# Kernel tuning notes

Measured on AMD Instinct MI355X. Metric: run time of the kernel, lower is better.

Reference implementation:

```python
import jax, jax.numpy as jnp
import numpy as np


def _rope(x, C):
    # x: [B, H, W, C]; 2 spatial channel dims -> k_max = C // 4
    B, H, W, _ = x.shape
    k_max = C // 4
    theta = 1.0 / (10000.0 ** (jnp.arange(k_max, dtype=x.dtype) / k_max))
    hh, ww = jnp.meshgrid(jnp.arange(H, dtype=x.dtype), jnp.arange(W, dtype=x.dtype), indexing='ij')
    angles = jnp.concatenate([hh[..., None] * theta, ww[..., None] * theta], axis=-1)  # [H, W, C//2]
    cos, sin = jnp.cos(angles), jnp.sin(angles)
    xr = x.reshape(B, H, W, C // 2, 2)
    x_re, x_im = xr[..., 0], xr[..., 1]
    out = jnp.stack([x_re * cos - x_im * sin, x_im * cos + x_re * sin], axis=-1)
    return out.reshape(B, H, W, C)


def _forward(x, W_qk, b_qk, scale_p, dwc_w, dwc_b, img_H, img_W):
    B, N, C = x.shape
    head_dim = dwc_w.shape[0]
    h = C // head_dim
    f = 3  # focusing_factor

    qk = x @ W_qk.T + b_qk                        # [B, N, 2C]
    q, k = qk[..., :C], qk[..., C:]
    v = x

    q = _rope(q.reshape(B, img_H, img_W, C), C).reshape(B, N, C)
    k = _rope(k.reshape(B, img_H, img_W, C), C).reshape(B, N, C)

    q = jax.nn.elu(q) + 1.0
    k = jax.nn.elu(k) + 1.0

    scale = jax.nn.softplus(scale_p)              # [1, 1, C]
    q = q / scale
    k = k / scale

    q_norm = jnp.linalg.norm(q, axis=-1, keepdims=True)
    k_norm = jnp.linalg.norm(k, axis=-1, keepdims=True)
    q = q ** f
    k = k ** f
    q = q / jnp.linalg.norm(q, axis=-1, keepdims=True) * q_norm
    k = k / jnp.linalg.norm(k, axis=-1, keepdims=True) * k_norm

    q = q.reshape(B, N, h, head_dim).transpose(0, 2, 1, 3)   # [B, h, N, d]
    k = k.reshape(B, N, h, head_dim).transpose(0, 2, 1, 3)
    v = v.reshape(B, N, h, head_dim).transpose(0, 2, 1, 3)

    k_mean = k.mean(axis=2, keepdims=True)                    # [B, h, 1, d]
    z = 1.0 / (jnp.einsum('bhnd,bhmd->bhnm', q, k_mean) + 1e-6)  # [B, h, N, 1]

    s = float(N) ** (-0.5)
    kv = jnp.einsum('bhnd,bhne->bhde', k * s, v * s)          # [B, h, d, d]
    out = jnp.einsum('bhnd,bhde->bhne', q, kv) * z            # [B, h, N, d]
    out = out.transpose(0, 2, 1, 3).reshape(B, N, C)

    # depthwise conv residual on v
    v_img = v.reshape(B * h, img_H, img_W, head_dim).transpose(0, 3, 1, 2)  # [B*h, d, H, W]
    conv = jax.lax.conv_general_dilated(
        v_img, dwc_w, window_strides=(1, 1), padding='SAME',
        dimension_numbers=('NCHW', 'OIHW', 'NCHW'),
        feature_group_count=head_dim) + dwc_b[None, :, None, None]
    out = out + conv.reshape(B, C, N).transpose(0, 2, 1)
    return out


def setup_inputs() -> dict:
    key = jax.random.key(0)
    ks = jax.random.split(key, 6)
    B, img_H, img_W, C, head_dim, ksz = 8, 64, 64, 512, 32, 5
    N = img_H * img_W
    x = jax.random.normal(ks[0], (B, N, C), dtype=jnp.float32)
    W_qk = jax.random.normal(ks[1], (2 * C, C), dtype=jnp.float32) * 0.02
    b_qk = jnp.zeros((2 * C,), dtype=jnp.float32)
    scale_p = jax.random.normal(ks[2], (1, 1, C), dtype=jnp.float32) * 0.02
    fan_out = ksz * ksz  # depthwise: out_channels/groups = 1
    dwc_w = jax.random.normal(ks[3], (head_dim, 1, ksz, ksz), dtype=jnp.float32) * np.sqrt(2.0 / fan_out)
    dwc_b = jnp.zeros((head_dim,), dtype=jnp.float32)
    return {"x": x, "W_qk": W_qk, "b_qk": b_qk, "scale_p": scale_p,
            "dwc_w": dwc_w, "dwc_b": dwc_b, "img_H": img_H, "img_W": img_W}


def reference(x, W_qk, b_qk, scale_p, dwc_w, dwc_b, img_H, img_W):
    return _forward(x, W_qk, b_qk, scale_p, dwc_w, dwc_b, img_H, img_W)
```

## Files before the change

kernel.cpp:

```cpp
#include <hip/hip_runtime.h>
#include <math.h>

#define B_SZ 8
#define IMG_H 64
#define IMG_W 64
#define N_TOK 4096
#define C_DIM 512
#define HEADS 16
#define HDIM 32
#define M_ROWS (B_SZ * N_TOK)
#define QK_COLS (2 * C_DIM)

#define THETA_COEF (-0.07195578415606394f)

typedef __attribute__((ext_vector_type(8))) __bf16 bf16x8;
typedef __attribute__((ext_vector_type(4))) float f32x4;

__device__ __forceinline__ void async_ld16(void* lds, const void* g) {
    __builtin_amdgcn_global_load_lds(
        (const __attribute__((address_space(1))) unsigned*)g,
        (__attribute__((address_space(3))) unsigned*)lds, 16, 0, 0);
}

__device__ __forceinline__ unsigned short f2bf(float f) {
    unsigned u = __float_as_uint(f);
    u += 0x7FFF + ((u >> 16) & 1);
    return (unsigned short)(u >> 16);
}

__global__ __launch_bounds__(256) void cvt_bf16_kernel(
    const float* __restrict__ src, unsigned short* __restrict__ dst)
{
    int i = blockIdx.x * 256 + threadIdx.x;
    float4 v = ((const float4*)src)[i];
    ushort4 o;
    o.x = f2bf(v.x); o.y = f2bf(v.y); o.z = f2bf(v.z); o.w = f2bf(v.w);
    ((ushort4*)dst)[i] = o;
}

__global__ __launch_bounds__(256) void rope_lut_kernel(
    const float* __restrict__ scale_p, float* __restrict__ lut)
{
    int idx = blockIdx.x * 256 + threadIdx.x;
    int pos = idx >> 7, tt = idx & 127;
    float theta = expf((float)tt * THETA_COEF);
    float ang = (float)pos * theta;
    lut[idx] = cosf(ang);
    lut[idx + 8192] = sinf(ang);
    if (idx < 512) lut[16384 + idx] = 1.0f / log1pf(expf(scale_p[idx]));
}

#define GBM 128
#define GBN 128
#define GBK 64

#define EPI_I(I, ACC) do {                                                    \
    float cr = cI, sr = sI;                                                   \
    _Pragma("unroll")                                                         \
    for (int r = 0; r < 4; ++r) {                                             \
        int m = m0 + wm + (I) * 16 + quad * 4 + r;                            \
        float val = (ACC)[r] + bias;                                          \
        float oth = __shfl_xor(val, 1);                                       \
        float rot = is_im ? (val * cr + oth * sr) : (val * cr - oth * sr);    \
        rot = (rot > 0.f) ? (rot + 1.f) : __expf(rot);                        \
        dst[(size_t)m * C_DIM + ch] = rot * rspv;                             \
        float tc = cr * c1 - sr * s1, ts = sr * c1 + cr * s1;                 \
        cr = tc; sr = ts;                                                     \
    }                                                                         \
    float uc = cI * c16 - sI * s16, us = sI * c16 + cI * s16;                 \
    cI = uc; sI = us;                                                         \
} while (0)

#define EPI_J(J, A0, A1, A2, A3) do {                                         \
    int c = n0 + wn + (J) * 16 + l16;                                         \
    int ch = c & 511;                                                         \
    float bias = bqk[c];                                                      \
    float rspv = rsp[ch];                                                     \
    int tt = ch >> 1;                                                         \
    int tl = tt & 127;                                                        \
    float cI, sI, c1, s1, c16, s16;                                           \
    if (tt < 128) {               \
        int pos = ((m0 + wm) & (N_TOK - 1)) >> 6;                             \
        cI = lut[pos * 128 + tl]; sI = lut[pos * 128 + tl + 8192];            \
        c1 = 1.f; s1 = 0.f; c16 = 1.f; s16 = 0.f;                             \
    } else {                  \
        int pos0 = quad * 4;                                                  \
        cI = lut[pos0 * 128 + tl]; sI = lut[pos0 * 128 + tl + 8192];          \
        c1  = lut[128 + tl];       s1  = lut[128 + tl + 8192];                \
        c16 = lut[2048 + tl];      s16 = lut[2048 + tl + 8192];               \
    }                                                                         \
    float* dst = (c < C_DIM) ? qW : kW;                                       \
    EPI_I(0, A0); EPI_I(1, A1); EPI_I(2, A2); EPI_I(3, A3);                   \
} while (0)

__global__ __launch_bounds__(256, 1) void gemm_mfma_kernel(
    const unsigned short* __restrict__ xb,
    const unsigned short* __restrict__ Wb,
    const float* __restrict__ bqk,
    const float* __restrict__ lut,
    float* __restrict__ qW,
    float* __restrict__ kW)
{
    __shared__ char lds[32768];
    char* As = lds;
    char* Bs = lds + 16384;

    const float* rsp = lut + 16384;

    const int t = threadIdx.x;
    const int wave = t >> 6;
    const int lane = t & 63;
    const int quad = lane >> 4;
    const int l16 = lane & 15;
    const int is_im = l16 & 1;

    const int flat = blockIdx.x + 8 * blockIdx.y;
    const int xcd = flat & 7;
    const int ii_ = flat >> 3;
    const int n0 = (ii_ & 7) * GBN;
    const int m0 = (xcd * 32 + (ii_ >> 3)) * GBM;

    const int wm = (wave >> 1) * 64;
    const int wn = (wave & 1) * 64;

    const int sr_ = t >> 3;
    const int ss_ = t & 7;

    f32x4 acc00 = {0.f,0.f,0.f,0.f}, acc01 = {0.f,0.f,0.f,0.f},
          acc02 = {0.f,0.f,0.f,0.f}, acc03 = {0.f,0.f,0.f,0.f},
          acc10 = {0.f,0.f,0.f,0.f}, acc11 = {0.f,0.f,0.f,0.f},
          acc12 = {0.f,0.f,0.f,0.f}, acc13 = {0.f,0.f,0.f,0.f},
          acc20 = {0.f,0.f,0.f,0.f}, acc21 = {0.f,0.f,0.f,0.f},
          acc22 = {0.f,0.f,0.f,0.f}, acc23 = {0.f,0.f,0.f,0.f},
          acc30 = {0.f,0.f,0.f,0.f}, acc31 = {0.f,0.f,0.f,0.f},
          acc32 = {0.f,0.f,0.f,0.f}, acc33 = {0.f,0.f,0.f,0.f};

    const int swz = (l16 >> 1) & 3;
    const int par = l16 & 1;

    for (int k0 = 0; k0 < C_DIM; k0 += GBK) {
        __syncthreads();
#pragma unroll
        for (int p = 0; p < 2; ++p) {
#pragma unroll
            for (int qq = 0; qq < 2; ++qq) {
                int r = qq * 32 + sr_;
                int j = ((ss_ & 3) ^ ((r >> 1) & 3)) | ((ss_ & 4) ^ ((r & 1) << 2));
                const unsigned short* ga =
                    xb + (size_t)(m0 + p * 64 + r) * C_DIM + k0 + j * 8;
                async_ld16(As + p * 8192 + qq * 4096 + wave * 1024, ga);
                const unsigned short* gb =
                    Wb + (size_t)(n0 + p * 64 + r) * C_DIM + k0 + j * 8;
                async_ld16(Bs + p * 8192 + qq * 4096 + wave * 1024, gb);
            }
        }
        __syncthreads();

#pragma unroll
        for (int kk = 0; kk < 2; ++kk) {
            const int co = ((quad ^ swz) + 4 * (kk ^ par)) * 16;
            bf16x8 a0 = *(const bf16x8*)(As + (wm + 0 * 16 + l16) * 128 + co);
            bf16x8 a1 = *(const bf16x8*)(As + (wm + 1 * 16 + l16) * 128 + co);
            bf16x8 a2 = *(const bf16x8*)(As + (wm + 2 * 16 + l16) * 128 + co);
            bf16x8 a3 = *(const bf16x8*)(As + (wm + 3 * 16 + l16) * 128 + co);
            bf16x8 b0 = *(const bf16x8*)(Bs + (wn + 0 * 16 + l16) * 128 + co);
            bf16x8 b1 = *(const bf16x8*)(Bs + (wn + 1 * 16 + l16) * 128 + co);
            bf16x8 b2 = *(const bf16x8*)(Bs + (wn + 2 * 16 + l16) * 128 + co);
            bf16x8 b3 = *(const bf16x8*)(Bs + (wn + 3 * 16 + l16) * 128 + co);

            acc00 = __builtin_amdgcn_mfma_f32_16x16x32_bf16(a0, b0, acc00, 0, 0, 0);
            acc01 = __builtin_amdgcn_mfma_f32_16x16x32_bf16(a0, b1, acc01, 0, 0, 0);
            acc02 = __builtin_amdgcn_mfma_f32_16x16x32_bf16(a0, b2, acc02, 0, 0, 0);
            acc03 = __builtin_amdgcn_mfma_f32_16x16x32_bf16(a0, b3, acc03, 0, 0, 0);
            acc10 = __builtin_amdgcn_mfma_f32_16x16x32_bf16(a1, b0, acc10, 0, 0, 0);
            acc11 = __builtin_amdgcn_mfma_f32_16x16x32_bf16(a1, b1, acc11, 0, 0, 0);
            acc12 = __builtin_amdgcn_mfma_f32_16x16x32_bf16(a1, b2, acc12, 0, 0, 0);
            acc13 = __builtin_amdgcn_mfma_f32_16x16x32_bf16(a1, b3, acc13, 0, 0, 0);
            acc20 = __builtin_amdgcn_mfma_f32_16x16x32_bf16(a2, b0, acc20, 0, 0, 0);
            acc21 = __builtin_amdgcn_mfma_f32_16x16x32_bf16(a2, b1, acc21, 0, 0, 0);
            acc22 = __builtin_amdgcn_mfma_f32_16x16x32_bf16(a2, b2, acc22, 0, 0, 0);
            acc23 = __builtin_amdgcn_mfma_f32_16x16x32_bf16(a2, b3, acc23, 0, 0, 0);
            acc30 = __builtin_amdgcn_mfma_f32_16x16x32_bf16(a3, b0, acc30, 0, 0, 0);
            acc31 = __builtin_amdgcn_mfma_f32_16x16x32_bf16(a3, b1, acc31, 0, 0, 0);
            acc32 = __builtin_amdgcn_mfma_f32_16x16x32_bf16(a3, b2, acc32, 0, 0, 0);
            acc33 = __builtin_amdgcn_mfma_f32_16x16x32_bf16(a3, b3, acc33, 0, 0, 0);
        }
    }

    EPI_J(0, acc00, acc10, acc20, acc30);
    EPI_J(1, acc01, acc11, acc21, acc31);
    EPI_J(2, acc02, acc12, acc22, acc32);
    EPI_J(3, acc03, acc13, acc23, acc33);
}

__global__ __launch_bounds__(256) void norm_kernel(
    const float* __restrict__ qW, const float* __restrict__ kW,
    float* __restrict__ sq, float* __restrict__ sk)
{
    int wave = threadIdx.x >> 6;
    int lane = threadIdx.x & 63;
    int m = blockIdx.x * 4 + wave;
    const float4* qr = (const float4*)(qW + (size_t)m * C_DIM);
    const float4* kr = (const float4*)(kW + (size_t)m * C_DIM);
    float q2 = 0.f, q6 = 0.f, k2 = 0.f, k6 = 0.f;
#pragma unroll
    for (int l = 0; l < 2; ++l) {
        float4 q4 = qr[lane + l * 64];
        float4 k4 = kr[lane + l * 64];
        float qq;
        qq = q4.x * q4.x; q2 += qq; q6 += qq * qq * qq;
        qq = q4.y * q4.y; q2 += qq; q6 += qq * qq * qq;
        qq = q4.z * q4.z; q2 += qq; q6 += qq * qq * qq;
        qq = q4.w * q4.w; q2 += qq; q6 += qq * qq * qq;
        qq = k4.x * k4.x; k2 += qq; k6 += qq * qq * qq;
        qq = k4.y * k4.y; k2 += qq; k6 += qq * qq * qq;
        qq = k4.z * k4.z; k2 += qq; k6 += qq * qq * qq;
        qq = k4.w * k4.w; k2 += qq; k6 += qq * qq * qq;
    }
#pragma unroll
    for (int off = 32; off > 0; off >>= 1) {
        q2 += __shfl_down(q2, off);
        q6 += __shfl_down(q6, off);
        k2 += __shfl_down(k2, off);
        k6 += __shfl_down(k6, off);
    }
    if (lane == 0) {
        sq[m] = sqrtf(q2) / sqrtf(q6);
        sk[m] = sqrtf(k2) / sqrtf(k6);
    }
}

#define NSPLIT 8
#define ROWS_PER_SPLIT (N_TOK / NSPLIT)

__global__ __launch_bounds__(256) void kv_partial_kernel(
    const float* __restrict__ x, const float* __restrict__ kW,
    const float* __restrict__ sk,
    float* __restrict__ kvp, float* __restrict__ kmp)
{
    int g = blockIdx.x >> 3;
    int split = blockIdx.x & 7;
    int b = g >> 4, h = g & 15;
    int n_start = split * ROWS_PER_SPLIT;

    __shared__ float smem[5120];
    float* kf = smem;
    float* vv = smem + 64 * 36;

    int t = threadIdx.x;
    int wave = t >> 6, lane = t & 63;
    int srow = t >> 3;
    int scol = (t & 7) * 4;
    int d0 = (lane >> 3) * 4;
    int e0 = (lane & 7) * 4;

    float acc[4][4] = {{0.f}};
    float4 kmacc = make_float4(0.f, 0.f, 0.f, 0.f);

    float4 kreg[2], vreg[2];
    float sreg[2];
#pragma unroll
    for (int h2 = 0; h2 < 2; ++h2) {
        int n = n_start + h2 * 32 + srow;
        size_t base = ((size_t)(b * N_TOK + n)) * C_DIM + h * HDIM + scol;
        kreg[h2] = *(const float4*)&kW[base];
        vreg[h2] = *(const float4*)&x[base];
        sreg[h2] = sk[b * N_TOK + n];
    }

    for (int tt = 0; tt < ROWS_PER_SPLIT / 64; ++tt) {
        __syncthreads();
#pragma unroll
        for (int h2 = 0; h2 < 2; ++h2) {
            int row = h2 * 32 + srow;
            float4 k4 = kreg[h2];
            float s = sreg[h2];
            float4 k3;
            k3.x = k4.x * k4.x * k4.x * s;
            k3.y = k4.y * k4.y * k4.y * s;
            k3.z = k4.z * k4.z * k4.z * s;
            k3.w = k4.w * k4.w * k4.w * s;
            *(float4*)&kf[row * 36 + scol] = k3;
            *(float4*)&vv[row * 36 + scol] = vreg[h2];
            kmacc.x += k3.x; kmacc.y += k3.y;
            kmacc.z += k3.z; kmacc.w += k3.w;
        }
        if (tt < ROWS_PER_SPLIT / 64 - 1) {
            int nb = n_start + (tt + 1) * 64;
#pragma unroll
            for (int h2 = 0; h2 < 2; ++h2) {
                int n = nb + h2 * 32 + srow;
                size_t base = ((size_t)(b * N_TOK + n)) * C_DIM + h * HDIM + scol;
                kreg[h2] = *(const float4*)&kW[base];
                vreg[h2] = *(const float4*)&x[base];
                sreg[h2] = sk[b * N_TOK + n];
            }
        }
        __syncthreads();

        const float* kfp = kf + (wave * 16) * 36 + d0;
        const float* vvp = vv + (wave * 16) * 36 + e0;
#pragma unroll
        for (int nn = 0; nn < 16; ++nn) {
            float4 k4 = *(const float4*)(kfp + nn * 36);
            float4 v4 = *(const float4*)(vvp + nn * 36);
            acc[0][0] += k4.x * v4.x; acc[0][1] += k4.x * v4.y;
            acc[0][2] += k4.x * v4.z; acc[0][3] += k4.x * v4.w;
            acc[1][0] += k4.y * v4.x; acc[1][1] += k4.y * v4.y;
            acc[1][2] += k4.y * v4.z; acc[1][3] += k4.y * v4.w;
            acc[2][0] += k4.z * v4.x; acc[2][1] += k4.z * v4.y;
            acc[2][2] += k4.z * v4.z; acc[2][3] += k4.z * v4.w;
            acc[3][0] += k4.w * v4.x; acc[3][1] += k4.w * v4.y;
            acc[3][2] += k4.w * v4.z; acc[3][3] += k4.w * v4.w;
        }
    }

    __syncthreads();
    float* red = smem;
    float* kmr = smem + 4096;
#pragma unroll
    for (int di = 0; di < 4; ++di) {
        float4 v = make_float4(acc[di][0], acc[di][1], acc[di][2], acc[di][3]);
        *(float4*)&red[wave * 1024 + (d0 + di) * 32 + e0] = v;
    }
    *(float4*)&kmr[srow * 32 + scol] = kmacc;
    __syncthreads();

    size_t pbase = (size_t)blockIdx.x * 1024;
    for (int idx = t; idx < 1024; idx += 256) {
        float s = red[idx] + red[1024 + idx] + red[2048 + idx] + red[3072 + idx];
        kvp[pbase + idx] = s;
    }
    if (t < 32) {
        float s = 0.f;
#pragma unroll
        for (int r = 0; r < 32; ++r) s += kmr[r * 32 + t];
        kmp[blockIdx.x * 32 + t] = s;
    }
}

__global__ __launch_bounds__(256) void kv_reduce_kernel(
    const float* __restrict__ kvp, const float* __restrict__ kmp,
    float* __restrict__ kv, float* __restrict__ km)
{
    int g = blockIdx.x;
    int t = threadIdx.x;
    for (int idx = t; idx < 1024; idx += 256) {
        float s = 0.f;
#pragma unroll
        for (int sp = 0; sp < NSPLIT; ++sp)
            s += kvp[((size_t)(g * NSPLIT + sp)) * 1024 + idx];
        int d = idx >> 5, e = idx & 31;
        kv[(size_t)g * 1024 + e * 32 + d] = s * (1.0f / 4096.0f);
    }
    if (t < 32) {
        float s = 0.f;
#pragma unroll
        for (int sp = 0; sp < NSPLIT; ++sp) s += kmp[(g * NSPLIT + sp) * 32 + t];
        km[g * 32 + t] = s * (1.0f / 4096.0f);
    }
}

__global__ __launch_bounds__(256) void attn_out_kernel(
    const float* __restrict__ qW, const float* __restrict__ sq,
    const float* __restrict__ kvT, const float* __restrict__ km,
    float* __restrict__ out)
{
    int g = blockIdx.x;
    int b = g >> 4, h = g & 15;
    int n0 = blockIdx.y * 128;

    __shared__ float qf[16][36];

    int t = threadIdx.x;
    int e = t & 15;
    int nl = t >> 4;
    int sd = e * 2;

    const float* kvg = kvT + (size_t)g * 1024;
    float4 kva[8], kvb[8], kmr[8];
#pragma unroll
    for (int j = 0; j < 8; ++j) {
        kva[j] = *(const float4*)&kvg[e * 32 + j * 4];
        kvb[j] = *(const float4*)&kvg[(e + 16) * 32 + j * 4];
        kmr[j] = *(const float4*)&km[g * 32 + j * 4];
    }

    size_t rbase = ((size_t)(b * N_TOK + n0 + nl)) * C_DIM + h * HDIM;

    float2 q2 = *(const float2*)&qW[rbase + sd];
    float sv = sq[b * N_TOK + n0 + nl];

    for (int ch = 0; ch < 8; ++ch) {
        __syncthreads();
        *(float2*)&qf[nl][sd] =
            make_float2(q2.x * q2.x * q2.x * sv, q2.y * q2.y * q2.y * sv);

        float2 q2n; float svn;
        if (ch < 7) {
            size_t nb = rbase + (size_t)(ch + 1) * 16 * C_DIM;
            q2n = *(const float2*)&qW[nb + sd];
            svn = sq[b * N_TOK + n0 + (ch + 1) * 16 + nl];
        }
        __syncthreads();

        float s1a = 0.f, s1b = 0.f, s2 = 0.f;
#pragma unroll
        for (int j = 0; j < 8; ++j) {
            float4 q4 = *(const float4*)&qf[nl][j * 4];
            s1a += q4.x * kva[j].x + q4.y * kva[j].y
                 + q4.z * kva[j].z + q4.w * kva[j].w;
            s1b += q4.x * kvb[j].x + q4.y * kvb[j].y
                 + q4.z * kvb[j].z + q4.w * kvb[j].w;
            s2  += q4.x * kmr[j].x + q4.y * kmr[j].y
                 + q4.z * kmr[j].z + q4.w * kmr[j].w;
        }
        float z = 1.0f / (s2 + 1e-6f);
        float* op = out + rbase + (size_t)ch * 16 * C_DIM;
        op[e] = s1a * z;
        op[e + 16] = s1b * z;

        if (ch < 7) { q2 = q2n; sv = svn; }
    }
}

__global__ __launch_bounds__(256, 2) void conv_kernel(
    const float* __restrict__ x, const float* __restrict__ w,
    const float* __restrict__ bias, float* __restrict__ out)
{
    __shared__ float wl[25][32];
    int t = threadIdx.x;
    for (int idx = t; idx < 800; idx += 256) {
        int o = idx & 31, tap = idx >> 5;
        wl[tap][o] = w[o * 25 + tap];
    }
    __syncthreads();

    int bi = blockIdx.x >> 3;
    int part = blockIdx.x & 7;
    int b = bi >> 6, i = bi & 63;
    int jg = part * 2 + (t >> 7);
    int cg = t & 127;
    int j0 = jg * 4;
    int o4 = (cg & 7) * 4;

    const float* xbase = x + ((size_t)b * N_TOK) * C_DIM + cg * 4;

    float4 b4 = *(const float4*)&bias[o4];
    float4 acc[4] = {b4, b4, b4, b4};

#pragma unroll
    for (int ki = 0; ki < 5; ++ki) {
        int ii = i + ki - 2;
        if (ii < 0 || ii >= IMG_H) continue;
        const float* xr = xbase + (size_t)ii * 64 * C_DIM;
        float4 row[8];
#pragma unroll
        for (int jx = 0; jx < 8; ++jx) {
            int jj = j0 + jx - 2;
            row[jx] = (jj >= 0 && jj < IMG_W)
                          ? *(const float4*)(xr + (size_t)jj * C_DIM)
                          : make_float4(0.f, 0.f, 0.f, 0.f);
        }
#pragma unroll
        for (int kj = 0; kj < 5; ++kj) {
            float4 w4 = *(const float4*)&wl[ki * 5 + kj][o4];
#pragma unroll
            for (int jo = 0; jo < 4; ++jo) {
                acc[jo].x += w4.x * row[jo + kj].x;
                acc[jo].y += w4.y * row[jo + kj].y;
                acc[jo].z += w4.z * row[jo + kj].z;
                acc[jo].w += w4.w * row[jo + kj].w;
            }
        }
    }

    float* op = out + ((size_t)(b * N_TOK + i * 64 + j0)) * C_DIM + cg * 4;
#pragma unroll
    for (int jo = 0; jo < 4; ++jo) {
        float4 cur = *(float4*)(op + (size_t)jo * C_DIM);
        cur.x += acc[jo].x;
        cur.y += acc[jo].y;
        cur.z += acc[jo].z;
        cur.w += acc[jo].w;
        *(float4*)(op + (size_t)jo * C_DIM) = cur;
    }
}

extern "C" void kernel_launch(void* const* d_in, const int* in_sizes, int n_in,
                              void* d_out, int out_size, void* d_ws, size_t ws_size,
                              hipStream_t stream) {
    const float* x       = (const float*)d_in[0];
    const float* Wqk     = (const float*)d_in[1];
    const float* bqk     = (const float*)d_in[2];
    const float* scale_p = (const float*)d_in[3];
    const float* dwc_w   = (const float*)d_in[4];
    const float* dwc_b   = (const float*)d_in[5];
    float* out = (float*)d_out;
    float* ws = (float*)d_ws;

    float* qW  = ws;
    float* sq  = qW + (size_t)M_ROWS * C_DIM;
    float* sk  = sq + M_ROWS;
    float* kvp = sk + M_ROWS;
    float* kmp = kvp + (size_t)1024 * 1024;
    float* kv  = kmp + 1024 * 32;
    float* km  = kv + 128 * 1024;
    unsigned short* xb = (unsigned short*)(km + 2048);
    unsigned short* Wb = xb + (size_t)M_ROWS * C_DIM;
    float* lut = (float*)(Wb + (size_t)QK_COLS * C_DIM);
    float* kW  = out;

    cvt_bf16_kernel<<<(M_ROWS * C_DIM) / 1024, 256, 0, stream>>>(x, xb);
    cvt_bf16_kernel<<<(QK_COLS * C_DIM) / 1024, 256, 0, stream>>>(Wqk, Wb);
    rope_lut_kernel<<<32, 256, 0, stream>>>(scale_p, lut);

    dim3 gg(QK_COLS / GBN, M_ROWS / GBM);
    gemm_mfma_kernel<<<gg, 256, 0, stream>>>(xb, Wb, bqk, lut, qW, kW);

    norm_kernel<<<M_ROWS / 4, 256, 0, stream>>>(qW, kW, sq, sk);

    kv_partial_kernel<<<128 * NSPLIT, 256, 0, stream>>>(x, kW, sk, kvp, kmp);
    kv_reduce_kernel<<<128, 256, 0, stream>>>(kvp, kmp, kv, km);

    dim3 g4(128, 32);
    attn_out_kernel<<<g4, 256, 0, stream>>>(qW, sq, kv, km, out);

    conv_kernel<<<M_ROWS / 8, 256, 0, stream>>>(x, dwc_w, dwc_b, out);
}
```

Baseline: 338.9 us.

## Double-buffer GEMM LDS tiles with GBK=32 and merge prep kernels

Rewrites the QK GEMM main loop to ping-pong between two 16KB LDS buffers of K-depth 32, so the async global-to-LDS load for the next tile is issued before the MFMAs on the current tile. This needs one barrier per iteration instead of two. Separately, the two bf16 conversion launches and the RoPE LUT launch are merged into one prep kernel to save launch overhead. The cost is twice as many loop iterations, each with less MFMA work to hide latency behind, plus a different LDS swizzle.

```diff
diff --git a/kernel.cpp b/kernel.cpp
--- a/kernel.cpp
+++ b/kernel.cpp
@@ -28,31 +28,40 @@
     return (unsigned short)(u >> 16);
 }
 
-__global__ __launch_bounds__(256) void cvt_bf16_kernel(
-    const float* __restrict__ src, unsigned short* __restrict__ dst)
-{
-    int i = blockIdx.x * 256 + threadIdx.x;
-    float4 v = ((const float4*)src)[i];
-    ushort4 o;
-    o.x = f2bf(v.x); o.y = f2bf(v.y); o.z = f2bf(v.z); o.w = f2bf(v.w);
-    ((ushort4*)dst)[i] = o;
-}
-
-__global__ __launch_bounds__(256) void rope_lut_kernel(
-    const float* __restrict__ scale_p, float* __restrict__ lut)
-{
-    int idx = blockIdx.x * 256 + threadIdx.x;
-    int pos = idx >> 7, tt = idx & 127;
-    float theta = expf((float)tt * THETA_COEF);
-    float ang = (float)pos * theta;
-    lut[idx] = cosf(ang);
-    lut[idx + 8192] = sinf(ang);
-    if (idx < 512) lut[16384 + idx] = 1.0f / log1pf(expf(scale_p[idx]));
+__global__ __launch_bounds__(256) void prep_kernel(
+    const float* __restrict__ x, const float* __restrict__ Wqk,
+    const float* __restrict__ scale_p,
+    unsigned short* __restrict__ xb, unsigned short* __restrict__ Wb,
+    float* __restrict__ lut)
+{
+    int bid = blockIdx.x;
+    int t = threadIdx.x;
+    if (bid < 16384) {
+        int i = bid * 256 + t;
+        float4 v = ((const float4*)x)[i];
+        ushort4 o;
+        o.x = f2bf(v.x); o.y = f2bf(v.y); o.z = f2bf(v.z); o.w = f2bf(v.w);
+        ((ushort4*)xb)[i] = o;
+    } else if (bid < 16896) {
+        int i = (bid - 16384) * 256 + t;
+        float4 v = ((const float4*)Wqk)[i];
+        ushort4 o;
+        o.x = f2bf(v.x); o.y = f2bf(v.y); o.z = f2bf(v.z); o.w = f2bf(v.w);
+        ((ushort4*)Wb)[i] = o;
+    } else {
+        int idx = (bid - 16896) * 256 + t;
+        int pos = idx >> 7, tt = idx & 127;
+        float theta = expf((float)tt * THETA_COEF);
+        float ang = (float)pos * theta;
+        lut[idx] = cosf(ang);
+        lut[idx + 8192] = sinf(ang);
+        if (idx < 512) lut[16384 + idx] = 1.0f / log1pf(expf(scale_p[idx]));
+    }
 }
 
 #define GBM 128
 #define GBN 128
-#define GBK 64
+#define GBK 32
 
 #define EPI_I(I, ACC) do {                                                    \
     float cr = cI, sr = sI;                                                   \
@@ -102,8 +111,6 @@
     float* __restrict__ kW)
 {
     __shared__ char lds[32768];
-    char* As = lds;
-    char* Bs = lds + 16384;
 
     const float* rsp = lut + 16384;
 
@@ -123,8 +130,8 @@
     const int wm = (wave >> 1) * 64;
     const int wn = (wave & 1) * 64;
 
-    const int sr_ = t >> 3;
-    const int ss_ = t & 7;
+    const int srow = t >> 2;
+    const int sj = t & 3;
 
     f32x4 acc00 = {0.f,0.f,0.f,0.f}, acc01 = {0.f,0.f,0.f,0.f},
           acc02 = {0.f,0.f,0.f,0.f}, acc03 = {0.f,0.f,0.f,0.f},
@@ -136,55 +143,57 @@
           acc32 = {0.f,0.f,0.f,0.f}, acc33 = {0.f,0.f,0.f,0.f};
 
     const int swz = (l16 >> 1) & 3;
-    const int par = l16 & 1;
+    const int co = (quad ^ swz) * 16;
+
+    auto stage = [&](int k0, int b) {
+#pragma unroll
+        for (int p = 0; p < 2; ++p) {
+            int m = p * 64 + srow;
+            int jp = sj ^ ((m >> 1) & 3);
+            const unsigned short* ga = xb + (size_t)(m0 + m) * C_DIM + k0 + jp * 8;
+            async_ld16(lds + b * 16384 + p * 4096 + wave * 1024, ga);
+            const unsigned short* gb = Wb + (size_t)(n0 + m) * C_DIM + k0 + jp * 8;
+            async_ld16(lds + b * 16384 + 8192 + p * 4096 + wave * 1024, gb);
+        }
+    };
+
+    stage(0, 0);
+    __syncthreads();
+    int buf = 0;
 
     for (int k0 = 0; k0 < C_DIM; k0 += GBK) {
+        if (k0 + GBK < C_DIM) stage(k0 + GBK, buf ^ 1);
+
+        const char* As = lds + buf * 16384;
+        const char* Bs = As + 8192;
+        bf16x8 a0 = *(const bf16x8*)(As + (wm + 0 * 16 + l16) * 64 + co);
+        bf16x8 a1 = *(const bf16x8*)(As + (wm + 1 * 16 + l16) * 64 + co);
+        bf16x8 a2 = *(const bf16x8*)(As + (wm + 2 * 16 + l16) * 64 + co);
+        bf16x8 a3 = *(const bf16x8*)(As + (wm + 3 * 16 + l16) * 64 + co);
+        bf16x8 b0 = *(const bf16x8*)(Bs + (wn + 0 * 16 + l16) * 64 + co);
+        bf16x8 b1 = *(const bf16x8*)(Bs + (wn + 1 * 16 + l16) * 64 + co);
+        bf16x8 b2 = *(const bf16x8*)(Bs + (wn + 2 * 16 + l16) * 64 + co);
+        bf16x8 b3 = *(const bf16x8*)(Bs + (wn + 3 * 16 + l16) * 64 + co);
+
+        acc00 = __builtin_amdgcn_mfma_f32_16x16x32_bf16(a0, b0, acc00, 0, 0, 0);
+        acc01 = __builtin_amdgcn_mfma_f32_16x16x32_bf16(a0, b1, acc01, 0, 0, 0);
+        acc02 = __builtin_amdgcn_mfma_f32_16x16x32_bf16(a0, b2, acc02, 0, 0, 0);
+        acc03 = __builtin_amdgcn_mfma_f32_16x16x32_bf16(a0, b3, acc03, 0, 0, 0);
+        acc10 = __builtin_amdgcn_mfma_f32_16x16x32_bf16(a1, b0, acc10, 0, 0, 0);
+        acc11 = __builtin_amdgcn_mfma_f32_16x16x32_bf16(a1, b1, acc11, 0, 0, 0);
+        acc12 = __builtin_amdgcn_mfma_f32_16x16x32_bf16(a1, b2, acc12, 0, 0, 0);
+        acc13 = __builtin_amdgcn_mfma_f32_16x16x32_bf16(a1, b3, acc13, 0, 0, 0);
+        acc20 = __builtin_amdgcn_mfma_f32_16x16x32_bf16(a2, b0, acc20, 0, 0, 0);
+        acc21 = __builtin_amdgcn_mfma_f32_16x16x32_bf16(a2, b1, acc21, 0, 0, 0);
+        acc22 = __builtin_amdgcn_mfma_f32_16x16x32_bf16(a2, b2, acc22, 0, 0, 0);
+        acc23 = __builtin_amdgcn_mfma_f32_16x16x32_bf16(a2, b3, acc23, 0, 0, 0);
+        acc30 = __builtin_amdgcn_mfma_f32_16x16x32_bf16(a3, b0, acc30, 0, 0, 0);
+        acc31 = __builtin_amdgcn_mfma_f32_16x16x32_bf16(a3, b1, acc31, 0, 0, 0);
+        acc32 = __builtin_amdgcn_mfma_f32_16x16x32_bf16(a3, b2, acc32, 0, 0, 0);
+        acc33 = __builtin_amdgcn_mfma_f32_16x16x32_bf16(a3, b3, acc33, 0, 0, 0);
+
         __syncthreads();
-#pragma unroll
-        for (int p = 0; p < 2; ++p) {
-#pragma unroll
-            for (int qq = 0; qq < 2; ++qq) {
-                int r = qq * 32 + sr_;
-                int j = ((ss_ & 3) ^ ((r >> 1) & 3)) | ((ss_ & 4) ^ ((r & 1) << 2));
-                const unsigned short* ga =
-                    xb + (size_t)(m0 + p * 64 + r) * C_DIM + k0 + j * 8;
-                async_ld16(As + p * 8192 + qq * 4096 + wave * 1024, ga);
-                const unsigned short* gb =
-                    Wb + (size_t)(n0 + p * 64 + r) * C_DIM + k0 + j * 8;
-                async_ld16(Bs + p * 8192 + qq * 4096 + wave * 1024, gb);
-            }
-        }
-        __syncthreads();
-
-#pragma unroll
-        for (int kk = 0; kk < 2; ++kk) {
-            const int co = ((quad ^ swz) + 4 * (kk ^ par)) * 16;
-            bf16x8 a0 = *(const bf16x8*)(As + (wm + 0 * 16 + l16) * 128 + co);
-            bf16x8 a1 = *(const bf16x8*)(As + (wm + 1 * 16 + l16) * 128 + co);
-            bf16x8 a2 = *(const bf16x8*)(As + (wm + 2 * 16 + l16) * 128 + co);
-            bf16x8 a3 = *(const bf16x8*)(As + (wm + 3 * 16 + l16) * 128 + co);
-            bf16x8 b0 = *(const bf16x8*)(Bs + (wn + 0 * 16 + l16) * 128 + co);
-            bf16x8 b1 = *(const bf16x8*)(Bs + (wn + 1 * 16 + l16) * 128 + co);
-            bf16x8 b2 = *(const bf16x8*)(Bs + (wn + 2 * 16 + l16) * 128 + co);
-            bf16x8 b3 = *(const bf16x8*)(Bs + (wn + 3 * 16 + l16) * 128 + co);
-
-            acc00 = __builtin_amdgcn_mfma_f32_16x16x32_bf16(a0, b0, acc00, 0, 0, 0);
-            acc01 = __builtin_amdgcn_mfma_f32_16x16x32_bf16(a0, b1, acc01, 0, 0, 0);
-            acc02 = __builtin_amdgcn_mfma_f32_16x16x32_bf16(a0, b2, acc02, 0, 0, 0);
-            acc03 = __builtin_amdgcn_mfma_f32_16x16x32_bf16(a0, b3, acc03, 0, 0, 0);
-            acc10 = __builtin_amdgcn_mfma_f32_16x16x32_bf16(a1, b0, acc10, 0, 0, 0);
-            acc11 = __builtin_amdgcn_mfma_f32_16x16x32_bf16(a1, b1, acc11, 0, 0, 0);
-            acc12 = __builtin_amdgcn_mfma_f32_16x16x32_bf16(a1, b2, acc12, 0, 0, 0);
-            acc13 = __builtin_amdgcn_mfma_f32_16x16x32_bf16(a1, b3, acc13, 0, 0, 0);
-            acc20 = __builtin_amdgcn_mfma_f32_16x16x32_bf16(a2, b0, acc20, 0, 0, 0);
-            acc21 = __builtin_amdgcn_mfma_f32_16x16x32_bf16(a2, b1, acc21, 0, 0, 0);
-            acc22 = __builtin_amdgcn_mfma_f32_16x16x32_bf16(a2, b2, acc22, 0, 0, 0);
-            acc23 = __builtin_amdgcn_mfma_f32_16x16x32_bf16(a2, b3, acc23, 0, 0, 0);
-            acc30 = __builtin_amdgcn_mfma_f32_16x16x32_bf16(a3, b0, acc30, 0, 0, 0);
-            acc31 = __builtin_amdgcn_mfma_f32_16x16x32_bf16(a3, b1, acc31, 0, 0, 0);
-            acc32 = __builtin_amdgcn_mfma_f32_16x16x32_bf16(a3, b2, acc32, 0, 0, 0);
-            acc33 = __builtin_amdgcn_mfma_f32_16x16x32_bf16(a3, b3, acc33, 0, 0, 0);
-        }
+        buf ^= 1;
     }
 
     EPI_J(0, acc00, acc10, acc20, acc30);
@@ -511,9 +520,7 @@
     float* lut = (float*)(Wb + (size_t)QK_COLS * C_DIM);
     float* kW  = out;
 
-    cvt_bf16_kernel<<<(M_ROWS * C_DIM) / 1024, 256, 0, stream>>>(x, xb);
-    cvt_bf16_kernel<<<(QK_COLS * C_DIM) / 1024, 256, 0, stream>>>(Wqk, Wb);
-    rope_lut_kernel<<<32, 256, 0, stream>>>(scale_p, lut);
+    prep_kernel<<<16928, 256, 0, stream>>>(x, Wqk, scale_p, xb, Wb, lut);
 
     dim3 gg(QK_COLS / GBN, M_ROWS / GBM);
     gemm_mfma_kernel<<<gg, 256, 0, stream>>>(xb, Wb, bqk, lut, qW, kW);
```

Measured after the change: 340.4 us. No clear change (+0.4%).
